# Kernel tuning notes

Measured on AMD Instinct MI355X. Metric: run time of the kernel, lower is better.

Reference implementation:

```python
import jax, jax.numpy as jnp
import numpy as np

B, V, F, L = 1024, 5023, 9976, 68
N_SHAPE, N_EXP, N_JOINTS = 100, 50, 5
PARENTS = np.array([-1, 0, 1, 1, 1])  # FLAME kintree: global, neck, jaw, eyeL, eyeR


def rodrigues(rv):
    # rv: [..., 3] axis-angle -> [..., 3, 3] rotation matrices
    angle = jnp.sqrt(jnp.sum(rv * rv, axis=-1, keepdims=True) + 1e-16)
    axis = rv / angle
    rx, ry, rz = axis[..., 0], axis[..., 1], axis[..., 2]
    z = jnp.zeros_like(rx)
    K = jnp.stack([z, -rz, ry, rz, z, -rx, -ry, rx, z], axis=-1).reshape(rv.shape[:-1] + (3, 3))
    s = jnp.sin(angle)[..., None]
    c = jnp.cos(angle)[..., None]
    I = jnp.eye(3, dtype=rv.dtype)
    return I + s * K + (1.0 - c) * (K @ K)


def setup_inputs() -> dict:
    key = jax.random.key(0)
    ks = jax.random.split(key, 16)
    inp = {
        "shape_params": jax.random.normal(ks[0], (B, N_SHAPE), jnp.float32),
        "expression_params": jax.random.normal(ks[1], (B, N_EXP), jnp.float32),
        "pose_params": 0.1 * jax.random.normal(ks[2], (B, 6), jnp.float32),
        "eye_pose_params": jnp.zeros((B, 6), jnp.float32),
        "translation": jax.random.normal(ks[3], (B, 3), jnp.float32),
        "v_template": jax.random.normal(ks[4], (V, 3), jnp.float32),
        "shapedirs": 0.01 * jax.random.normal(ks[5], (V, 3, N_SHAPE + N_EXP), jnp.float32),
        "posedirs": 0.01 * jax.random.normal(ks[6], (9 * (N_JOINTS - 1), V * 3), jnp.float32),
        "J_regressor": jax.random.uniform(ks[7], (N_JOINTS, V), jnp.float32) / V,
        "lbs_weights": jax.nn.softmax(jax.random.normal(ks[8], (V, N_JOINTS), jnp.float32), axis=-1),
        "faces": jax.random.randint(ks[9], (F, 3), 0, V),
        "lmk_faces_idx": jax.random.randint(ks[10], (L,), 0, F),
    }
    bc = jax.random.uniform(ks[11], (L, 3), jnp.float32)
    inp["lmk_bary_coords"] = bc / jnp.sum(bc, axis=-1, keepdims=True)
    return inp


def reference(shape_params, expression_params, pose_params, eye_pose_params, translation,
              v_template, shapedirs, posedirs, J_regressor, lbs_weights,
              faces, lmk_faces_idx, lmk_bary_coords):
    Bn = shape_params.shape[0]
    dtype = shape_params.dtype
    # 1) shape + expression blendshapes
    betas = jnp.concatenate([shape_params, expression_params], axis=-1)          # [B,150]
    v_shaped = v_template + jnp.einsum('bl,vcl->bvc', betas, shapedirs)          # [B,V,3]
    J = jnp.einsum('jv,bvc->bjc', J_regressor, v_shaped)                         # [B,5,3]
    # 3) full pose: global + neck(zeros) + jaw + two eyes
    neck = jnp.zeros((Bn, 3), dtype)
    full_pose = jnp.concatenate([pose_params[:, :3], neck, pose_params[:, 3:6],
                                 eye_pose_params], axis=1).reshape(Bn, N_JOINTS, 3)
    rot_mats = rodrigues(full_pose)                                              # [B,5,3,3]
    # 4) pose blendshapes (driven by non-root rotations minus identity)
    I3 = jnp.eye(3, dtype=dtype)
    pose_feature = (rot_mats[:, 1:] - I3).reshape(Bn, -1)                        # [B,36]
    v_posed = v_shaped + (pose_feature @ posedirs).reshape(Bn, V, 3)             # [B,V,3]
    # 5) kinematic chain of rigid transforms
    rel_j = jnp.concatenate([J[:, :1], J[:, 1:] - J[:, PARENTS[1:]]], axis=1)    # [B,5,3]
    T_local = jnp.zeros((Bn, N_JOINTS, 4, 4), dtype)
    T_local = (T_local.at[..., :3, :3].set(rot_mats)
                      .at[..., :3, 3].set(rel_j)
                      .at[..., 3, 3].set(1.0))
    A = [T_local[:, 0]]
    for j in range(1, N_JOINTS):  # fixed tiny chain (5 joints)
        A.append(A[int(PARENTS[j])] @ T_local[:, j])
    A = jnp.stack(A, axis=1)                                                     # [B,5,4,4]
    # remove rest-pose joint locations from translations
    A_rel = A.at[..., :3, 3].add(-jnp.einsum('bjmn,bjn->bjm', A[..., :3, :3], J))
    # 6) linear blend skinning (only the 3x4 part is needed)
    T = jnp.einsum('vj,bjmn->bvmn', lbs_weights, A_rel[:, :, :3, :])             # [B,V,3,4]
    verts = jnp.einsum('bvmn,bvn->bvm', T[..., :3], v_posed) + T[..., 3]
    verts = verts + translation[:, None, :]
    # 7) barycentric landmark gather
    lmk_faces = faces[lmk_faces_idx]                                             # [L,3]
    lmk_verts = verts[:, lmk_faces]                                              # [B,L,3,3]
    landmarks = jnp.einsum('blfi,lf->bli', lmk_verts, lmk_bary_coords)           # [B,L,3]
    return jnp.concatenate([verts, landmarks], axis=1)                           # [B,V+L,3]
```

## Files before the change

kernel.cpp:

```cpp
#include <hip/hip_runtime.h>
#include <math.h>

#define BN 1024
#define NV 5023
#define NL 68
#define NVP 5088
#define NPL 15264
#define OSTR 15273
#define KTOT 192
#define NG 24

typedef unsigned short u16;
typedef short bf16x8 __attribute__((ext_vector_type(8)));
typedef u16 u16x8 __attribute__((ext_vector_type(8)));
typedef float f32x4 __attribute__((ext_vector_type(4)));

#define O_JSX  0
#define O_PART 4096
#define O_AREL 200704
#define O_EH   262144
#define O_EL   360448
#define O_GH   458752
#define O_GL   1924096

__device__ __forceinline__ u16 f2bf(float x) {
  unsigned u = __float_as_uint(x);
  return (u16)((u + 0x7FFFu + ((u >> 16) & 1u)) >> 16);
}
__device__ __forceinline__ float bf2f(u16 h) {
  return __uint_as_float(((unsigned)h) << 16);
}

__global__ __launch_bounds__(256) void k0(const float* __restrict__ sd,
                                          const float* __restrict__ pd,
                                          const float* __restrict__ vt,
                                          const float* __restrict__ jreg,
                                          float* __restrict__ part,
                                          u16* __restrict__ gph,
                                          u16* __restrict__ gpl) {
  __shared__ float ldsT[64 * 208];
  __shared__ float jr[320];
  const int tid = threadIdx.x;
  const int v0 = blockIdx.x * 64;
  const int c = blockIdx.y;
  for (int idx = tid; idx < 64 * 150; idx += 256) {
    int vv = idx / 150, k = idx - vv * 150;
    int v = v0 + vv;
    ldsT[vv * 208 + k] = (v < NV) ? sd[((size_t)v * 3 + c) * 150 + k] : 0.f;
  }
  for (int idx = tid; idx < 36 * 64; idx += 256) {
    int kk = idx >> 6, vv = idx & 63;
    int v = v0 + vv;
    ldsT[vv * 208 + 150 + kk] = (v < NV) ? pd[(size_t)kk * 15069 + (size_t)v * 3 + c] : 0.f;
  }
  for (int idx = tid; idx < 64 * 6; idx += 256) {
    int vv = idx / 6, kk = idx - vv * 6;
    int v = v0 + vv;
    ldsT[vv * 208 + 186 + kk] = (kk == 0 && v < NV) ? vt[(size_t)v * 3 + c] : 0.f;
  }
  for (int idx = tid; idx < 320; idx += 256) {
    int j = idx >> 6, vv = idx & 63;
    int v = v0 + vv;
    jr[idx] = (v < NV) ? jreg[(size_t)j * NV + v] : 0.f;
  }
  __syncthreads();
  if (tid < 192) {
    int k = tid;
    float s0 = 0.f, s1 = 0.f, s2 = 0.f, s3 = 0.f, s4 = 0.f;
    for (int vv = 0; vv < 64; ++vv) {
      float x = ldsT[vv * 208 + k];
      s0 = fmaf(jr[vv], x, s0);
      s1 = fmaf(jr[64 + vv], x, s1);
      s2 = fmaf(jr[128 + vv], x, s2);
      s3 = fmaf(jr[192 + vv], x, s3);
      s4 = fmaf(jr[256 + vv], x, s4);
    }
    int km = (k < 150) ? k : ((k == 186) ? 150 : -1);
    if (km >= 0) {
      size_t base = ((size_t)blockIdx.x * 15 + c) * 160;
      part[base + 0 * 480 + km] = s0;
      part[base + 1 * 480 + km] = s1;
      part[base + 2 * 480 + km] = s2;
      part[base + 3 * 480 + km] = s3;
      part[base + 4 * 480 + km] = s4;
    }
  }
  {
    int q = tid >> 6, vv = tid & 63;
    int v = v0 + vv;
    if (v < NVP) {
#pragma unroll
      for (int gg = 0; gg < 6; ++gg) {
        int g = q * 6 + gg;
        u16x8 h8, l8;
#pragma unroll
        for (int j = 0; j < 8; ++j) {
          float x = ldsT[vv * 208 + g * 8 + j];
          u16 h = f2bf(x);
          h8[j] = h;
          l8[j] = f2bf(x - bf2f(h));
        }
        size_t off = ((size_t)g * NPL + (size_t)c * NVP + v) * 8;
        *(u16x8*)(gph + off) = h8;
        *(u16x8*)(gpl + off) = l8;
      }
    }
  }
}

__global__ void k1b(const float* __restrict__ part, float* __restrict__ jsx) {
  int jc = blockIdx.x, k = threadIdx.x;
  if (k < 151) {
    float s = 0.f;
    for (int vch = 0; vch < 80; ++vch)
      s += part[((size_t)vch * 15 + jc) * 160 + k];
    jsx[jc * 152 + k] = s;
  }
}

__global__ __launch_bounds__(64) void k2(const float* __restrict__ shp,
                                         const float* __restrict__ expr,
                                         const float* __restrict__ pose,
                                         const float* __restrict__ eye,
                                         const float* __restrict__ jsx,
                                         u16* __restrict__ eph,
                                         u16* __restrict__ epl,
                                         float* __restrict__ arel) {
  int b = blockIdx.x, t = threadIdx.x;
  __shared__ float bet[150];
  __shared__ float Rm[5][9];
  __shared__ float Tl[5][16];
  __shared__ float Am[5][16];
  __shared__ float Jl[15];
  for (int i = t; i < 150; i += 64)
    bet[i] = (i < 100) ? shp[b * 100 + i] : expr[b * 50 + (i - 100)];
  __syncthreads();
  if (t < 60) {
    int jc = t >> 2, sub = t & 3;
    float acc = 0.f;
    for (int m = 0; m < 38; ++m) {
      int l = sub + 4 * m;
      if (l < 150) acc += jsx[jc * 152 + l] * bet[l];
      else if (l == 150) acc += jsx[jc * 152 + 150];
    }
    acc += __shfl_xor(acc, 1);
    acc += __shfl_xor(acc, 2);
    if (sub == 0) Jl[jc] = acc;
  }
  __syncthreads();
  if (t < 5) {
    float r0, r1, r2;
    if (t == 0)      { r0 = pose[b*6+0]; r1 = pose[b*6+1]; r2 = pose[b*6+2]; }
    else if (t == 2) { r0 = pose[b*6+3]; r1 = pose[b*6+4]; r2 = pose[b*6+5]; }
    else if (t == 3) { r0 = eye[b*6+0];  r1 = eye[b*6+1];  r2 = eye[b*6+2];  }
    else if (t == 4) { r0 = eye[b*6+3];  r1 = eye[b*6+4];  r2 = eye[b*6+5];  }
    else             { r0 = 0.f; r1 = 0.f; r2 = 0.f; }
    float ang = sqrtf(r0*r0 + r1*r1 + r2*r2 + 1e-16f);
    float ax = r0/ang, ay = r1/ang, az = r2/ang;
    float s = sinf(ang), cc = cosf(ang), o = 1.f - cc;
    float R0 = 1.f - o*(ay*ay+az*az);
    float R1 = -s*az + o*ax*ay;
    float R2 =  s*ay + o*ax*az;
    float R3 =  s*az + o*ax*ay;
    float R4 = 1.f - o*(ax*ax+az*az);
    float R5 = -s*ax + o*ay*az;
    float R6 = -s*ay + o*ax*az;
    float R7 =  s*ax + o*ay*az;
    float R8 = 1.f - o*(ax*ax+ay*ay);
    Rm[t][0]=R0; Rm[t][1]=R1; Rm[t][2]=R2; Rm[t][3]=R3; Rm[t][4]=R4;
    Rm[t][5]=R5; Rm[t][6]=R6; Rm[t][7]=R7; Rm[t][8]=R8;
    int par = (t == 0) ? -1 : ((t == 1) ? 0 : 1);
    float j0 = Jl[t*3+0], j1 = Jl[t*3+1], j2 = Jl[t*3+2];
    if (par >= 0) { j0 -= Jl[par*3+0]; j1 -= Jl[par*3+1]; j2 -= Jl[par*3+2]; }
    Tl[t][0]=R0; Tl[t][1]=R1; Tl[t][2]=R2;  Tl[t][3]=j0;
    Tl[t][4]=R3; Tl[t][5]=R4; Tl[t][6]=R5;  Tl[t][7]=j1;
    Tl[t][8]=R6; Tl[t][9]=R7; Tl[t][10]=R8; Tl[t][11]=j2;
    Tl[t][12]=0.f; Tl[t][13]=0.f; Tl[t][14]=0.f; Tl[t][15]=1.f;
  }
  __syncthreads();
  if (t < 16) Am[0][t] = Tl[0][t];
  __syncthreads();
  if (t < 16) {
    int m = t / 4, n = t % 4;
    float s = 0.f;
#pragma unroll
    for (int k = 0; k < 4; ++k) s += Am[0][m*4+k] * Tl[1][k*4+n];
    Am[1][t] = s;
  }
  __syncthreads();
  if (t < 48) {
    int jj = 2 + t / 16, tt = t % 16;
    int m = tt / 4, n = tt % 4;
    float s = 0.f;
#pragma unroll
    for (int k = 0; k < 4; ++k) s += Am[1][m*4+k] * Tl[jj][k*4+n];
    Am[jj][tt] = s;
  }
  __syncthreads();
  if (t < 60) {
    int j = t / 12, rr = (t % 12) / 4, cc = t % 4;
    float val = Am[j][rr*4+cc];
    if (cc == 3)
      val = Am[j][rr*4+3] - (Am[j][rr*4+0]*Jl[j*3+0] + Am[j][rr*4+1]*Jl[j*3+1] + Am[j][rr*4+2]*Jl[j*3+2]);
    arel[b * 60 + t] = val;
  }
  for (int k = t; k < 192; k += 64) {
    float val;
    if (k < 150) val = bet[k];
    else if (k < 186) {
      int kk = k - 150;
      int j = kk / 9 + 1, rc = kk % 9;
      val = Rm[j][rc] - ((rc == 0 || rc == 4 || rc == 8) ? 1.f : 0.f);
    } else if (k == 186) val = 1.f;
    else val = 0.f;
    u16 h = f2bf(val);
    u16 lo = f2bf(val - bf2f(h));
    int g = k >> 3, j8 = k & 7;
    eph[((size_t)g * 1024 + b) * 8 + j8] = h;
    epl[((size_t)g * 1024 + b) * 8 + j8] = lo;
  }
}

__global__ __launch_bounds__(512, 2) void k3(const u16* __restrict__ eph,
                                             const u16* __restrict__ epl,
                                             const u16* __restrict__ gph,
                                             const u16* __restrict__ gpl,
                                             const float* __restrict__ arel,
                                             const float* __restrict__ w,
                                             const float* __restrict__ tr,
                                             float* __restrict__ outp) {
  __shared__ __align__(16) float sAr[128 * 68];
  __shared__ float sTr[128 * 4];
  const int tid = threadIdx.x;
  const int lane = tid & 63, wave = tid >> 6;
  const int wr = wave >> 2, wc = wave & 3;
  const int l15 = lane & 15, g0 = lane >> 4;
  const int b_blk = blockIdx.y * 128;
  const int vglob = blockIdx.x * 64 + wc * 16 + l15;

  f32x4 acc[4][3];
#pragma unroll
  for (int mt = 0; mt < 4; ++mt)
#pragma unroll
    for (int c = 0; c < 3; ++c) { acc[mt][c][0]=0.f; acc[mt][c][1]=0.f; acc[mt][c][2]=0.f; acc[mt][c][3]=0.f; }

  size_t aoff = ((size_t)g0 * 1024 + (size_t)(b_blk + wr * 64 + l15)) * 8;
  size_t boff = ((size_t)g0 * NPL + (size_t)vglob) * 8;

#pragma unroll 2
  for (int ks = 0; ks < 6; ++ks) {
    bf16x8 ah[4], al[4], bh[3], bl[3];
#pragma unroll
    for (int mt = 0; mt < 4; ++mt) {
      ah[mt] = *(const bf16x8*)(eph + aoff + mt * 128);
      al[mt] = *(const bf16x8*)(epl + aoff + mt * 128);
    }
#pragma unroll
    for (int c = 0; c < 3; ++c) {
      bh[c] = *(const bf16x8*)(gph + boff + (size_t)c * (NVP * 8));
      bl[c] = *(const bf16x8*)(gpl + boff + (size_t)c * (NVP * 8));
    }
#pragma unroll
    for (int c = 0; c < 3; ++c)
#pragma unroll
      for (int mt = 0; mt < 4; ++mt) {
        acc[mt][c] = __builtin_amdgcn_mfma_f32_16x16x32_bf16(ah[mt], bh[c], acc[mt][c], 0, 0, 0);
        acc[mt][c] = __builtin_amdgcn_mfma_f32_16x16x32_bf16(ah[mt], bl[c], acc[mt][c], 0, 0, 0);
        acc[mt][c] = __builtin_amdgcn_mfma_f32_16x16x32_bf16(al[mt], bh[c], acc[mt][c], 0, 0, 0);
      }
    aoff += (size_t)4 * 1024 * 8;
    boff += (size_t)4 * NPL * 8;
  }

  for (int idx = tid; idx < 128 * 60; idx += 512) {
    int bb = idx / 60, r = idx - bb * 60;
    sAr[bb * 68 + r] = arel[(size_t)(b_blk + bb) * 60 + r];
  }
  for (int idx = tid; idx < 384; idx += 512) {
    int bb = idx / 3;
    sTr[bb * 4 + (idx - bb * 3)] = tr[(size_t)b_blk * 3 + idx];
  }
  __syncthreads();

  int v_c = vglob < NV ? vglob : NV - 1;
  float wreg[5];
#pragma unroll
  for (int j = 0; j < 5; ++j) wreg[j] = w[(size_t)v_c * 5 + j];

#pragma unroll
  for (int mt = 0; mt < 4; ++mt) {
#pragma unroll
    for (int r = 0; r < 4; ++r) {
      int bl_ = wr * 64 + mt * 16 + g0 * 4 + r;
      const float4* Ar = (const float4*)(sAr + bl_ * 68);
      float4 T0 = {0.f,0.f,0.f,0.f}, T1 = {0.f,0.f,0.f,0.f}, T2 = {0.f,0.f,0.f,0.f};
#pragma unroll
      for (int j = 0; j < 5; ++j) {
        float wj = wreg[j];
        float4 x = Ar[j * 3 + 0], y = Ar[j * 3 + 1], z = Ar[j * 3 + 2];
        T0.x = fmaf(wj, x.x, T0.x); T0.y = fmaf(wj, x.y, T0.y);
        T0.z = fmaf(wj, x.z, T0.z); T0.w = fmaf(wj, x.w, T0.w);
        T1.x = fmaf(wj, y.x, T1.x); T1.y = fmaf(wj, y.y, T1.y);
        T1.z = fmaf(wj, y.z, T1.z); T1.w = fmaf(wj, y.w, T1.w);
        T2.x = fmaf(wj, z.x, T2.x); T2.y = fmaf(wj, z.y, T2.y);
        T2.z = fmaf(wj, z.z, T2.z); T2.w = fmaf(wj, z.w, T2.w);
      }
      float px = acc[mt][0][r], py = acc[mt][1][r], pz = acc[mt][2][r];
      float ox = fmaf(T0.x, px, fmaf(T0.y, py, fmaf(T0.z, pz, T0.w + sTr[bl_ * 4 + 0])));
      float oy = fmaf(T1.x, px, fmaf(T1.y, py, fmaf(T1.z, pz, T1.w + sTr[bl_ * 4 + 1])));
      float oz = fmaf(T2.x, px, fmaf(T2.y, py, fmaf(T2.z, pz, T2.w + sTr[bl_ * 4 + 2])));
      if (vglob < NV) {
        float* op = outp + (size_t)(b_blk + bl_) * OSTR + (size_t)vglob * 3;
        op[0] = ox; op[1] = oy; op[2] = oz;
      }
    }
  }
}

__global__ void k4(const int* __restrict__ faces, const int* __restrict__ lfi,
                   const float* __restrict__ bary, float* __restrict__ outp) {
  int idx = blockIdx.x * 256 + threadIdx.x;
  if (idx >= BN * NL * 3) return;
  int b = idx / (NL * 3), rem = idx % (NL * 3);
  int l = rem / 3, i = rem % 3;
  int fi = lfi[l];
  float s = 0.f;
#pragma unroll
  for (int f = 0; f < 3; ++f) {
    int vid = faces[fi * 3 + f];
    s += bary[l * 3 + f] * outp[(size_t)b * OSTR + (size_t)vid * 3 + i];
  }
  outp[(size_t)b * OSTR + (size_t)(NV + l) * 3 + i] = s;
}

extern "C" void kernel_launch(void* const* d_in, const int* in_sizes, int n_in,
                              void* d_out, int out_size, void* d_ws, size_t ws_size,
                              hipStream_t stream) {
  const float* shp  = (const float*)d_in[0];
  const float* expr = (const float*)d_in[1];
  const float* pose = (const float*)d_in[2];
  const float* eye  = (const float*)d_in[3];
  const float* tr   = (const float*)d_in[4];
  const float* vt   = (const float*)d_in[5];
  const float* sd   = (const float*)d_in[6];
  const float* pd   = (const float*)d_in[7];
  const float* jreg = (const float*)d_in[8];
  const float* w    = (const float*)d_in[9];
  const int* faces  = (const int*)d_in[10];
  const int* lfi    = (const int*)d_in[11];
  const float* bary = (const float*)d_in[12];
  float* ws = (float*)d_ws;
  float* jsx  = ws + O_JSX;
  float* part = ws + O_PART;
  float* arel = ws + O_AREL;
  u16* eph = (u16*)(ws + O_EH);
  u16* epl = (u16*)(ws + O_EL);
  u16* gph = (u16*)(ws + O_GH);
  u16* gpl = (u16*)(ws + O_GL);
  float* outp = (float*)d_out;

  k0<<<dim3(80, 3), 256, 0, stream>>>(sd, pd, vt, jreg, part, gph, gpl);
  k1b<<<15, 160, 0, stream>>>(part, jsx);
  k2<<<1024, 64, 0, stream>>>(shp, expr, pose, eye, jsx, eph, epl, arel);
  k3<<<dim3(79, 8), 512, 0, stream>>>(eph, epl, gph, gpl, arel, w, tr, outp);
  k4<<<816, 256, 0, stream>>>(faces, lfi, bary, outp);
}
```

Measured before the change: 93.24 us.

## Restructure skinning GEMM with vertex-major tiles, transposed weights, LDS-free epilogue

The blendshape MFMA kernel swaps operand roles: vertices now form the M tiles and batch the N columns. It runs 256-thread blocks on an 80x16 grid, and padded vertices now reach a 64-multiple (5120). The setup kernel writes a vertex-contiguous transposed copy of the skinning weights. The epilogue drops the LDS staging of joint transforms and translation, and instead reads each lane's batch row directly from global memory and blends per joint. Accumulators are split into a main part and a correction part, and a lo*lo MFMA is added. This adds matrix work and epilogue FLOPs, and output stores now stride across batch rows, which may hurt coalescing.

```diff
diff --git a/kernel.cpp b/kernel.cpp
--- a/kernel.cpp
+++ b/kernel.cpp
@@ -4,8 +4,8 @@
 #define BN 1024
 #define NV 5023
 #define NL 68
-#define NVP 5088
-#define NPL 15264
+#define NVP 5120
+#define NPL 15360
 #define OSTR 15273
 #define KTOT 192
 #define NG 24
@@ -17,11 +17,12 @@
 
 #define O_JSX  0
 #define O_PART 4096
+#define O_EH   4096
+#define O_EL   102400
 #define O_AREL 200704
-#define O_EH   262144
-#define O_EL   360448
-#define O_GH   458752
-#define O_GL   1924096
+#define O_WT   262144
+#define O_GH   294912
+#define O_GL   1769472
 
 __device__ __forceinline__ u16 f2bf(float x) {
   unsigned u = __float_as_uint(x);
@@ -35,7 +36,9 @@
                                           const float* __restrict__ pd,
                                           const float* __restrict__ vt,
                                           const float* __restrict__ jreg,
+                                          const float* __restrict__ w,
                                           float* __restrict__ part,
+                                          float* __restrict__ wT,
                                           u16* __restrict__ gph,
                                           u16* __restrict__ gpl) {
   __shared__ float ldsT[64 * 208];
@@ -62,6 +65,13 @@
     int j = idx >> 6, vv = idx & 63;
     int v = v0 + vv;
     jr[idx] = (v < NV) ? jreg[(size_t)j * NV + v] : 0.f;
+  }
+  if (c == 0) {
+    for (int idx = tid; idx < 320; idx += 256) {
+      int vv = idx / 5, j = idx - vv * 5;
+      int v = v0 + vv;
+      wT[(size_t)j * NVP + v] = (v < NV) ? w[(size_t)v * 5 + j] : 0.f;
+    }
   }
   __syncthreads();
   if (tid < 192) {
@@ -88,22 +98,20 @@
   {
     int q = tid >> 6, vv = tid & 63;
     int v = v0 + vv;
-    if (v < NVP) {
-#pragma unroll
-      for (int gg = 0; gg < 6; ++gg) {
-        int g = q * 6 + gg;
-        u16x8 h8, l8;
-#pragma unroll
-        for (int j = 0; j < 8; ++j) {
-          float x = ldsT[vv * 208 + g * 8 + j];
-          u16 h = f2bf(x);
-          h8[j] = h;
-          l8[j] = f2bf(x - bf2f(h));
-        }
-        size_t off = ((size_t)g * NPL + (size_t)c * NVP + v) * 8;
-        *(u16x8*)(gph + off) = h8;
-        *(u16x8*)(gpl + off) = l8;
-      }
+#pragma unroll
+    for (int gg = 0; gg < 6; ++gg) {
+      int g = q * 6 + gg;
+      u16x8 h8, l8;
+#pragma unroll
+      for (int j = 0; j < 8; ++j) {
+        float x = ldsT[vv * 208 + g * 8 + j];
+        u16 h = f2bf(x);
+        h8[j] = h;
+        l8[j] = f2bf(x - bf2f(h));
+      }
+      size_t off = ((size_t)g * NPL + (size_t)c * NVP + v) * 8;
+      *(u16x8*)(gph + off) = h8;
+      *(u16x8*)(gpl + off) = l8;
     }
   }
 }
@@ -221,97 +229,92 @@
   }
 }
 
-__global__ __launch_bounds__(512, 2) void k3(const u16* __restrict__ eph,
+__global__ __launch_bounds__(256, 3) void k3(const u16* __restrict__ eph,
                                              const u16* __restrict__ epl,
                                              const u16* __restrict__ gph,
                                              const u16* __restrict__ gpl,
                                              const float* __restrict__ arel,
-                                             const float* __restrict__ w,
+                                             const float* __restrict__ wT,
                                              const float* __restrict__ tr,
                                              float* __restrict__ outp) {
-  __shared__ __align__(16) float sAr[128 * 68];
-  __shared__ float sTr[128 * 4];
   const int tid = threadIdx.x;
-  const int lane = tid & 63, wave = tid >> 6;
-  const int wr = wave >> 2, wc = wave & 3;
+  const int lane = tid & 63, wb = tid >> 6;
   const int l15 = lane & 15, g0 = lane >> 4;
-  const int b_blk = blockIdx.y * 128;
-  const int vglob = blockIdx.x * 64 + wc * 16 + l15;
-
-  f32x4 acc[4][3];
+  const int vbase = blockIdx.x * 64;
+  const int bcol = blockIdx.y * 64 + wb * 16 + l15;
+
+  f32x4 accb[4][3], accs[4][3];
 #pragma unroll
   for (int mt = 0; mt < 4; ++mt)
 #pragma unroll
-    for (int c = 0; c < 3; ++c) { acc[mt][c][0]=0.f; acc[mt][c][1]=0.f; acc[mt][c][2]=0.f; acc[mt][c][3]=0.f; }
-
-  size_t aoff = ((size_t)g0 * 1024 + (size_t)(b_blk + wr * 64 + l15)) * 8;
-  size_t boff = ((size_t)g0 * NPL + (size_t)vglob) * 8;
-
-#pragma unroll 2
+    for (int c = 0; c < 3; ++c)
+#pragma unroll
+      for (int r = 0; r < 4; ++r) { accb[mt][c][r] = 0.f; accs[mt][c][r] = 0.f; }
+
+  size_t aoff = ((size_t)g0 * NPL + (size_t)(vbase + l15)) * 8;
+  size_t boff = ((size_t)g0 * 1024 + (size_t)bcol) * 8;
+
   for (int ks = 0; ks < 6; ++ks) {
-    bf16x8 ah[4], al[4], bh[3], bl[3];
-#pragma unroll
-    for (int mt = 0; mt < 4; ++mt) {
-      ah[mt] = *(const bf16x8*)(eph + aoff + mt * 128);
-      al[mt] = *(const bf16x8*)(epl + aoff + mt * 128);
-    }
+    bf16x8 bh = *(const bf16x8*)(eph + boff);
+    bf16x8 bl = *(const bf16x8*)(epl + boff);
 #pragma unroll
     for (int c = 0; c < 3; ++c) {
-      bh[c] = *(const bf16x8*)(gph + boff + (size_t)c * (NVP * 8));
-      bl[c] = *(const bf16x8*)(gpl + boff + (size_t)c * (NVP * 8));
-    }
-#pragma unroll
-    for (int c = 0; c < 3; ++c)
+      bf16x8 ah[4], al[4];
 #pragma unroll
       for (int mt = 0; mt < 4; ++mt) {
-        acc[mt][c] = __builtin_amdgcn_mfma_f32_16x16x32_bf16(ah[mt], bh[c], acc[mt][c], 0, 0, 0);
-        acc[mt][c] = __builtin_amdgcn_mfma_f32_16x16x32_bf16(ah[mt], bl[c], acc[mt][c], 0, 0, 0);
-        acc[mt][c] = __builtin_amdgcn_mfma_f32_16x16x32_bf16(al[mt], bh[c], acc[mt][c], 0, 0, 0);
-      }
-    aoff += (size_t)4 * 1024 * 8;
-    boff += (size_t)4 * NPL * 8;
-  }
-
-  for (int idx = tid; idx < 128 * 60; idx += 512) {
-    int bb = idx / 60, r = idx - bb * 60;
-    sAr[bb * 68 + r] = arel[(size_t)(b_blk + bb) * 60 + r];
-  }
-  for (int idx = tid; idx < 384; idx += 512) {
-    int bb = idx / 3;
-    sTr[bb * 4 + (idx - bb * 3)] = tr[(size_t)b_blk * 3 + idx];
-  }
-  __syncthreads();
-
-  int v_c = vglob < NV ? vglob : NV - 1;
-  float wreg[5];
-#pragma unroll
-  for (int j = 0; j < 5; ++j) wreg[j] = w[(size_t)v_c * 5 + j];
+        ah[mt] = *(const bf16x8*)(gph + aoff + (size_t)c * (NVP * 8) + mt * 128);
+        al[mt] = *(const bf16x8*)(gpl + aoff + (size_t)c * (NVP * 8) + mt * 128);
+      }
+#pragma unroll
+      for (int mt = 0; mt < 4; ++mt) {
+        accb[mt][c] = __builtin_amdgcn_mfma_f32_16x16x32_bf16(ah[mt], bh, accb[mt][c], 0, 0, 0);
+        accs[mt][c] = __builtin_amdgcn_mfma_f32_16x16x32_bf16(ah[mt], bl, accs[mt][c], 0, 0, 0);
+        accs[mt][c] = __builtin_amdgcn_mfma_f32_16x16x32_bf16(al[mt], bh, accs[mt][c], 0, 0, 0);
+        accs[mt][c] = __builtin_amdgcn_mfma_f32_16x16x32_bf16(al[mt], bl, accs[mt][c], 0, 0, 0);
+      }
+    }
+    aoff += (size_t)NPL * 32;
+    boff += (size_t)1024 * 32;
+  }
+
+  const float t0 = tr[(size_t)bcol * 3 + 0];
+  const float t1 = tr[(size_t)bcol * 3 + 1];
+  const float t2 = tr[(size_t)bcol * 3 + 2];
+  const float4* ar4 = (const float4*)(arel + (size_t)bcol * 60);
 
 #pragma unroll
   for (int mt = 0; mt < 4; ++mt) {
+    const int v4 = vbase + mt * 16 + g0 * 4;
+    float o0[4], o1[4], o2[4];
+#pragma unroll
+    for (int r = 0; r < 4; ++r) { o0[r] = t0; o1[r] = t1; o2[r] = t2; }
+#pragma unroll
+    for (int j = 0; j < 5; ++j) {
+      float4 a0 = ar4[j * 3 + 0];
+      float4 a1 = ar4[j * 3 + 1];
+      float4 a2 = ar4[j * 3 + 2];
+      float4 wj = *(const float4*)(wT + (size_t)j * NVP + v4);
+      float wjr[4] = {wj.x, wj.y, wj.z, wj.w};
+#pragma unroll
+      for (int r = 0; r < 4; ++r) {
+        float px = accb[mt][0][r] + accs[mt][0][r];
+        float py = accb[mt][1][r] + accs[mt][1][r];
+        float pz = accb[mt][2][r] + accs[mt][2][r];
+        float yx = fmaf(a0.x, px, fmaf(a0.y, py, fmaf(a0.z, pz, a0.w)));
+        float yy = fmaf(a1.x, px, fmaf(a1.y, py, fmaf(a1.z, pz, a1.w)));
+        float yz = fmaf(a2.x, px, fmaf(a2.y, py, fmaf(a2.z, pz, a2.w)));
+        o0[r] = fmaf(wjr[r], yx, o0[r]);
+        o1[r] = fmaf(wjr[r], yy, o1[r]);
+        o2[r] = fmaf(wjr[r], yz, o2[r]);
+      }
+    }
+    float* op = outp + (size_t)bcol * OSTR + (size_t)v4 * 3;
 #pragma unroll
     for (int r = 0; r < 4; ++r) {
-      int bl_ = wr * 64 + mt * 16 + g0 * 4 + r;
-      const float4* Ar = (const float4*)(sAr + bl_ * 68);
-      float4 T0 = {0.f,0.f,0.f,0.f}, T1 = {0.f,0.f,0.f,0.f}, T2 = {0.f,0.f,0.f,0.f};
-#pragma unroll
-      for (int j = 0; j < 5; ++j) {
-        float wj = wreg[j];
-        float4 x = Ar[j * 3 + 0], y = Ar[j * 3 + 1], z = Ar[j * 3 + 2];
-        T0.x = fmaf(wj, x.x, T0.x); T0.y = fmaf(wj, x.y, T0.y);
-        T0.z = fmaf(wj, x.z, T0.z); T0.w = fmaf(wj, x.w, T0.w);
-        T1.x = fmaf(wj, y.x, T1.x); T1.y = fmaf(wj, y.y, T1.y);
-        T1.z = fmaf(wj, y.z, T1.z); T1.w = fmaf(wj, y.w, T1.w);
-        T2.x = fmaf(wj, z.x, T2.x); T2.y = fmaf(wj, z.y, T2.y);
-        T2.z = fmaf(wj, z.z, T2.z); T2.w = fmaf(wj, z.w, T2.w);
-      }
-      float px = acc[mt][0][r], py = acc[mt][1][r], pz = acc[mt][2][r];
-      float ox = fmaf(T0.x, px, fmaf(T0.y, py, fmaf(T0.z, pz, T0.w + sTr[bl_ * 4 + 0])));
-      float oy = fmaf(T1.x, px, fmaf(T1.y, py, fmaf(T1.z, pz, T1.w + sTr[bl_ * 4 + 1])));
-      float oz = fmaf(T2.x, px, fmaf(T2.y, py, fmaf(T2.z, pz, T2.w + sTr[bl_ * 4 + 2])));
-      if (vglob < NV) {
-        float* op = outp + (size_t)(b_blk + bl_) * OSTR + (size_t)vglob * 3;
-        op[0] = ox; op[1] = oy; op[2] = oz;
+      if (v4 + r < NV) {
+        op[r * 3 + 0] = o0[r];
+        op[r * 3 + 1] = o1[r];
+        op[r * 3 + 2] = o2[r];
       }
     }
   }
@@ -353,15 +356,16 @@
   float* jsx  = ws + O_JSX;
   float* part = ws + O_PART;
   float* arel = ws + O_AREL;
+  float* wT   = ws + O_WT;
   u16* eph = (u16*)(ws + O_EH);
   u16* epl = (u16*)(ws + O_EL);
   u16* gph = (u16*)(ws + O_GH);
   u16* gpl = (u16*)(ws + O_GL);
   float* outp = (float*)d_out;
 
-  k0<<<dim3(80, 3), 256, 0, stream>>>(sd, pd, vt, jreg, part, gph, gpl);
+  k0<<<dim3(80, 3), 256, 0, stream>>>(sd, pd, vt, jreg, w, part, wT, gph, gpl);
   k1b<<<15, 160, 0, stream>>>(part, jsx);
   k2<<<1024, 64, 0, stream>>>(shp, expr, pose, eye, jsx, eph, epl, arel);
-  k3<<<dim3(79, 8), 512, 0, stream>>>(eph, epl, gph, gpl, arel, w, tr, outp);
+  k3<<<dim3(80, 16), 256, 0, stream>>>(eph, epl, gph, gpl, arel, wT, tr, outp);
   k4<<<816, 256, 0, stream>>>(faces, lfi, bary, outp);
 }
```

After: 149.4 us. +60.2%, slower.
